# Kernel tuning notes

Measured on AMD Instinct MI355X. Metric: run time of the kernel, lower is better.

## Reference

```python
import jax, jax.numpy as jnp
import numpy as np

B, S, D, H = 4, 2048, 768, 12
HD = D // H  # head_dim = 64
NEG = 1e10
EPS = 1e-5

def setup_inputs() -> dict:
    key = jax.random.key(0)
    k1, k2, k3 = jax.random.split(key, 3)
    return {
        "context": jax.random.normal(k1, (B, S, D), dtype=jnp.float32),
        "pad_mask": jnp.ones((B, S), dtype=jnp.float32),
        "w_qkv": jax.random.normal(k2, (D, 3 * D), dtype=jnp.float32) * 0.02,
        "w_proj": jax.random.normal(k3, (D, D), dtype=jnp.float32) * (0.02 / np.sqrt(2.0 * 12)),
        "b_proj": jnp.zeros((D,), dtype=jnp.float32),
        "gamma": jnp.ones((D,), dtype=jnp.float32),
        "beta": jnp.zeros((D,), dtype=jnp.float32),
    }

def reference(context, pad_mask, w_qkv, w_proj, b_proj, gamma, beta):
    b, s, d = context.shape
    resid = context
    qkv = context @ w_qkv                       # [B,S,3D]
    q, k, v = jnp.split(qkv, 3, axis=-1)
    # [B,S,D] -> [B,H,S,HD]
    q = q.reshape(b, s, H, HD).transpose(0, 2, 1, 3)
    k = k.reshape(b, s, H, HD).transpose(0, 2, 1, 3)
    v = v.reshape(b, s, H, HD).transpose(0, 2, 1, 3)
    scores = jnp.einsum("bhqd,bhkd->bhqk", q, k) * (1.0 / np.sqrt(HD))
    m = pad_mask[:, None, None, :]              # [B,1,1,S]
    scores = scores * m - (1.0 - m) * NEG       # multiplicative mask + big negative
    attn = jax.nn.softmax(scores, axis=-1)      # dropout is identity at inference
    out = jnp.einsum("bhqk,bhkd->bhqd", attn, v)
    out = out.transpose(0, 2, 1, 3).reshape(b, s, d)
    out = out @ w_proj + b_proj
    x = out + resid
    mu = jnp.mean(x, axis=-1, keepdims=True)
    var = jnp.var(x, axis=-1, keepdims=True)
    return (x - mu) * jax.lax.rsqrt(var + EPS) * gamma + beta
```

## Files before the change

kernel.cpp:

```cpp
#include <hip/hip_runtime.h>

#define BB 4
#define SS 2048
#define DD 768
#define HH 12
#define HDD 64
#define BS (BB*SS)
#define NQKV (3*DD)
#define NEL (BS*DD)

typedef __attribute__((ext_vector_type(8))) __bf16 bf16x8;
typedef __attribute__((ext_vector_type(4))) float fx4;
typedef __attribute__((ext_vector_type(4))) int   ix4;

#define MFMA16(a,b,c) __builtin_amdgcn_mfma_f32_16x16x32_bf16((a),(b),(c),0,0,0)

#define GLLDS(g, l) __builtin_amdgcn_global_load_lds( \
    (const __attribute__((address_space(1))) void*)(g), \
    (__attribute__((address_space(3))) void*)(l), 16, 0, 0)

__device__ __forceinline__ unsigned short f2bf(float f) {
  unsigned u = __builtin_bit_cast(unsigned, f);
  u = (u + 0x7FFFu + ((u >> 16) & 1u)) >> 16;
  return (unsigned short)u;
}
__device__ __forceinline__ unsigned pkbf(float a, float b) {
  unsigned ua = __builtin_bit_cast(unsigned, a);
  unsigned ub = __builtin_bit_cast(unsigned, b);
  return ((ua + 0x8000u) >> 16) | ((ub + 0x8000u) & 0xFFFF0000u);
}
__device__ __forceinline__ unsigned cvtpk(float a, float b) {
  unsigned r;
  asm("v_cvt_pk_bf16_f32 %0, %1, %2" : "=v"(r) : "v"(a), "v"(b));
  return r;
}
__device__ __forceinline__ float ex2(float x) { return __builtin_amdgcn_exp2f(x); }

__global__ __launch_bounds__(256) void pack_bf16(const float* __restrict__ x,
                                                 unsigned short* __restrict__ y, int n4) {
  int i = blockIdx.x * 256 + threadIdx.x;
  if (i < n4) {
    float4 v = ((const float4*)x)[i];
    ((uint2*)y)[i] = make_uint2(pkbf(v.x, v.y), pkbf(v.z, v.w));
  }
}

__global__ __launch_bounds__(256) void mask_coef_k(const float* __restrict__ m,
                                                   float* __restrict__ ka,
                                                   float* __restrict__ kb, int n) {
  int i = blockIdx.x * 256 + threadIdx.x;
  if (i < n) {
    float v = m[i];
    ka[i] = v * 0.18033688f;
    kb[i] = __builtin_fmaf(v, 1.44269504e10f, -1.44269504e10f);
  }
}

__global__ __launch_bounds__(256) void pack_transpose(const float* __restrict__ w,
                                                      unsigned short* __restrict__ wT,
                                                      int K, int N) {
  __shared__ unsigned short t[32][33];
  int n0 = blockIdx.x * 32, k0 = blockIdx.y * 32;
  int tx = threadIdx.x & 31, ty = threadIdx.x >> 5;
#pragma unroll
  for (int r = ty; r < 32; r += 8)
    t[tx][r] = f2bf(w[(size_t)(k0 + r) * N + n0 + tx]);
  __syncthreads();
#pragma unroll
  for (int r = ty; r < 32; r += 8)
    wT[(size_t)(n0 + r) * K + k0 + tx] = t[r][tx];
}

__global__ __launch_bounds__(256) void gemm_qkv_k(const unsigned short* __restrict__ Wt,
                                                  const unsigned short* __restrict__ X,
                                                  unsigned short* __restrict__ Qo,
                                                  unsigned short* __restrict__ Ko,
                                                  unsigned short* __restrict__ Vto) {
  __shared__ unsigned short As[2 * 128 * 32];
  __shared__ unsigned short Bs[2 * 128 * 32];
  const int tid = threadIdx.x;
  const int w = tid >> 6, lane = tid & 63, quad = lane >> 4, l16 = lane & 15;
  const int m0 = blockIdx.y << 7;
  const int n0 = blockIdx.x << 7;
  const int wm = (w & 1) * 64, wn = (w >> 1) * 64;
  fx4 acc[4][4];
#pragma unroll
  for (int i = 0; i < 4; ++i)
#pragma unroll
    for (int c = 0; c < 4; ++c) acc[i][c] = (fx4){0.f, 0.f, 0.f, 0.f};

  const int c0 = tid, c1 = 256 + tid;
  const unsigned short* Ag0 = Wt + (size_t)(m0 + (c0 >> 2)) * DD + (c0 & 3) * 8;
  const unsigned short* Ag1 = Wt + (size_t)(m0 + (c1 >> 2)) * DD + (c1 & 3) * 8;
  const unsigned short* Bg0 = X + (size_t)(n0 + (c0 >> 2)) * DD + (c0 & 3) * 8;
  const unsigned short* Bg1 = X + (size_t)(n0 + (c1 >> 2)) * DD + (c1 & 3) * 8;
  const int wb = w * 1024;

  GLLDS(Ag0, (char*)As + wb);
  GLLDS(Ag1, (char*)As + 4096 + wb);
  GLLDS(Bg0, (char*)Bs + wb);
  GLLDS(Bg1, (char*)Bs + 4096 + wb);
  int cur = 0;

  for (int k0 = 0; k0 < DD; k0 += 32) {
    __syncthreads();
    if (k0 + 32 < DD) {
      GLLDS(Ag0 + k0 + 32, (char*)As + (cur ^ 1) * 8192 + wb);
      GLLDS(Ag1 + k0 + 32, (char*)As + (cur ^ 1) * 8192 + 4096 + wb);
      GLLDS(Bg0 + k0 + 32, (char*)Bs + (cur ^ 1) * 8192 + wb);
      GLLDS(Bg1 + k0 + 32, (char*)Bs + (cur ^ 1) * 8192 + 4096 + wb);
    }
    const unsigned short* Asc = As + cur * 4096;
    const unsigned short* Bsc = Bs + cur * 4096;
    bf16x8 af[4], bf[4];
#pragma unroll
    for (int i = 0; i < 4; ++i) af[i] = *(const bf16x8*)&Asc[(wm + i * 16 + l16) * 32 + quad * 8];
#pragma unroll
    for (int c = 0; c < 4; ++c) bf[c] = *(const bf16x8*)&Bsc[(wn + c * 16 + l16) * 32 + quad * 8];
#pragma unroll
    for (int i = 0; i < 4; ++i)
#pragma unroll
      for (int c = 0; c < 4; ++c) acc[i][c] = MFMA16(af[i], bf[c], acc[i][c]);
    cur ^= 1;
  }

  const int which = m0 / DD;
#pragma unroll
  for (int i = 0; i < 4; ++i) {
    int fb = m0 + wm + i * 16 + quad * 4;
    int d = fb - which * DD;
    int h = d >> 6, hd = d & 63;
#pragma unroll
    for (int c = 0; c < 4; ++c) {
      int srow = n0 + wn + c * 16 + l16;
      int b = srow >> 11, s = srow & (SS - 1);
      if (which == 0) {
        uint2 v = make_uint2(pkbf(acc[i][c][0], acc[i][c][1]), pkbf(acc[i][c][2], acc[i][c][3]));
        *(uint2*)&Qo[((size_t)(b * HH + h) * SS + s) * HDD + hd] = v;
      } else if (which == 1) {
        uint2 v = make_uint2(pkbf(acc[i][c][0], acc[i][c][1]), pkbf(acc[i][c][2], acc[i][c][3]));
        *(uint2*)&Ko[((size_t)(b * HH + h) * SS + s) * HDD + hd] = v;
      } else {
#pragma unroll
        for (int r = 0; r < 4; ++r)
          Vto[((size_t)(b * HH + h) * HDD + hd + r) * SS + s] = f2bf(acc[i][c][r]);
      }
    }
  }
}

__global__ __launch_bounds__(256) void gemm_proj_k(const unsigned short* __restrict__ Wt,
                                                   const unsigned short* __restrict__ X,
                                                   const float* __restrict__ ctx,
                                                   const float* __restrict__ bproj,
                                                   float* __restrict__ xf) {
  __shared__ unsigned short As[2 * 128 * 32];
  __shared__ unsigned short Bs[2 * 128 * 32];
  const int tid = threadIdx.x;
  const int w = tid >> 6, lane = tid & 63, quad = lane >> 4, l16 = lane & 15;
  const int m0 = blockIdx.y << 7;
  const int n0 = blockIdx.x << 7;
  const int wm = (w & 1) * 64, wn = (w >> 1) * 64;
  fx4 acc[4][4];
#pragma unroll
  for (int i = 0; i < 4; ++i)
#pragma unroll
    for (int c = 0; c < 4; ++c) acc[i][c] = (fx4){0.f, 0.f, 0.f, 0.f};

  const int c0 = tid, c1 = 256 + tid;
  const unsigned short* Ag0 = Wt + (size_t)(m0 + (c0 >> 2)) * DD + (c0 & 3) * 8;
  const unsigned short* Ag1 = Wt + (size_t)(m0 + (c1 >> 2)) * DD + (c1 & 3) * 8;
  const unsigned short* Bg0 = X + (size_t)(n0 + (c0 >> 2)) * DD + (c0 & 3) * 8;
  const unsigned short* Bg1 = X + (size_t)(n0 + (c1 >> 2)) * DD + (c1 & 3) * 8;
  const int wb = w * 1024;

  GLLDS(Ag0, (char*)As + wb);
  GLLDS(Ag1, (char*)As + 4096 + wb);
  GLLDS(Bg0, (char*)Bs + wb);
  GLLDS(Bg1, (char*)Bs + 4096 + wb);
  int cur = 0;

  for (int k0 = 0; k0 < DD; k0 += 32) {
    __syncthreads();
    if (k0 + 32 < DD) {
      GLLDS(Ag0 + k0 + 32, (char*)As + (cur ^ 1) * 8192 + wb);
      GLLDS(Ag1 + k0 + 32, (char*)As + (cur ^ 1) * 8192 + 4096 + wb);
      GLLDS(Bg0 + k0 + 32, (char*)Bs + (cur ^ 1) * 8192 + wb);
      GLLDS(Bg1 + k0 + 32, (char*)Bs + (cur ^ 1) * 8192 + 4096 + wb);
    }
    const unsigned short* Asc = As + cur * 4096;
    const unsigned short* Bsc = Bs + cur * 4096;
    bf16x8 af[4], bf[4];
#pragma unroll
    for (int i = 0; i < 4; ++i) af[i] = *(const bf16x8*)&Asc[(wm + i * 16 + l16) * 32 + quad * 8];
#pragma unroll
    for (int c = 0; c < 4; ++c) bf[c] = *(const bf16x8*)&Bsc[(wn + c * 16 + l16) * 32 + quad * 8];
#pragma unroll
    for (int i = 0; i < 4; ++i)
#pragma unroll
      for (int c = 0; c < 4; ++c) acc[i][c] = MFMA16(af[i], bf[c], acc[i][c]);
    cur ^= 1;
  }

#pragma unroll
  for (int i = 0; i < 4; ++i) {
    int fb = m0 + wm + i * 16 + quad * 4;
    float4 bp = *(const float4*)&bproj[fb];
#pragma unroll
    for (int c = 0; c < 4; ++c) {
      int srow = n0 + wn + c * 16 + l16;
      float4 cx = *(const float4*)&ctx[(size_t)srow * DD + fb];
      float4 r;
      r.x = acc[i][c][0] + bp.x + cx.x;
      r.y = acc[i][c][1] + bp.y + cx.y;
      r.z = acc[i][c][2] + bp.z + cx.z;
      r.w = acc[i][c][3] + bp.w + cx.w;
      *(float4*)&xf[(size_t)srow * DD + fb] = r;
    }
  }
}

__global__ __launch_bounds__(256) void attn_k(const unsigned short* __restrict__ Q,
                                              const unsigned short* __restrict__ K,
                                              const unsigned short* __restrict__ Vt,
                                              const float* __restrict__ ka,
                                              const float* __restrict__ kb,
                                              unsigned short* __restrict__ O) {
  __shared__ unsigned short Ks[64 * 64];
  __shared__ unsigned short Vts[64 * 64];
  __shared__ float kaS[SS];
  __shared__ float kbS[SS];
  const int tid = threadIdx.x;
  const int w = tid >> 6, lane = tid & 63;
  const int quad = lane >> 4, l16 = lane & 15;
  const int bh = blockIdx.y;
  const int b = bh / HH, h = bh - b * HH;
  const int q0 = blockIdx.x << 7;
  const unsigned short* Qb = Q + (size_t)bh * (SS * HDD);
  const unsigned short* Kb = K + (size_t)bh * (SS * HDD);
  const unsigned short* Vtb = Vt + (size_t)bh * (SS * HDD);
  const float* ka_b = ka + b * SS;
  const float* kb_b = kb + b * SS;

#pragma unroll
  for (int i = 0; i < 2; ++i) {
    int idx = i * 256 + tid;
    ((float4*)kaS)[idx] = ((const float4*)ka_b)[idx];
    ((float4*)kbS)[idx] = ((const float4*)kb_b)[idx];
  }

  bf16x8 qf[2][2];
#pragma unroll
  for (int qi = 0; qi < 2; ++qi)
#pragma unroll
    for (int f = 0; f < 2; ++f)
      qf[qi][f] = *(const bf16x8*)&Qb[(size_t)(q0 + w * 32 + qi * 16 + l16) * HDD + f * 32 + quad * 8];

  fx4 o[2][4];
#pragma unroll
  for (int qi = 0; qi < 2; ++qi)
#pragma unroll
    for (int ht = 0; ht < 4; ++ht) o[qi][ht] = (fx4){0.f, 0.f, 0.f, 0.f};
  fx4 sacc[2];
  sacc[0] = (fx4){0.f, 0.f, 0.f, 0.f};
  sacc[1] = (fx4){0.f, 0.f, 0.f, 0.f};

  const ix4 one4 = (ix4){0x3F803F80, 0x3F803F80, 0x3F803F80, 0x3F803F80};
  const bf16x8 onesf = __builtin_bit_cast(bf16x8, one4);

  const int cA = tid, cB = 256 + tid;
  const int rA = cA >> 3, pA = (cA & 7) ^ (rA & 7);
  const int rB = cB >> 3, pB = (cB & 7) ^ (rB & 7);

  ix4 rk0 = *(const ix4*)&Kb[(size_t)rA * HDD + pA * 8];
  ix4 rk1 = *(const ix4*)&Kb[(size_t)rB * HDD + pB * 8];
  ix4 rv0 = *(const ix4*)&Vtb[(size_t)rA * SS + pA * 8];
  ix4 rv1 = *(const ix4*)&Vtb[(size_t)rB * SS + pB * 8];

  for (int k0 = 0; k0 < SS; k0 += 64) {
    __syncthreads();
    *(ix4*)((char*)Ks + cA * 16) = rk0;
    *(ix4*)((char*)Ks + cB * 16) = rk1;
    *(ix4*)((char*)Vts + cA * 16) = rv0;
    *(ix4*)((char*)Vts + cB * 16) = rv1;
    __syncthreads();
    if (k0 + 64 < SS) {
      int kn = k0 + 64;
      rk0 = *(const ix4*)&Kb[(size_t)(kn + rA) * HDD + pA * 8];
      rk1 = *(const ix4*)&Kb[(size_t)(kn + rB) * HDD + pB * 8];
      rv0 = *(const ix4*)&Vtb[(size_t)rA * SS + kn + pA * 8];
      rv1 = *(const ix4*)&Vtb[(size_t)rB * SS + kn + pB * 8];
    }

    float4 mqa[4], mqb[4];
#pragma unroll
    for (int kt = 0; kt < 4; ++kt) {
      mqa[kt] = *(const float4*)&kaS[k0 + kt * 16 + quad * 4];
      mqb[kt] = *(const float4*)&kbS[k0 + kt * 16 + quad * 4];
    }

    bf16x8 kf[4][2];
#pragma unroll
    for (int kt = 0; kt < 4; ++kt) {
      int row = kt * 16 + l16;
      int rx = row & 7;
#pragma unroll
      for (int f = 0; f < 2; ++f)
        kf[kt][f] = *(const bf16x8*)&Ks[row * 64 + ((f * 4 + quad) ^ rx) * 8];
    }
    bf16x8 vf[4][2];
#pragma unroll
    for (int ht = 0; ht < 4; ++ht) {
      int row = ht * 16 + l16;
      int rx = row & 7;
#pragma unroll
      for (int f = 0; f < 2; ++f) {
        int dc0 = (f * 4 + (quad >> 1)) ^ rx;
        int dc1 = (f * 4 + 2 + (quad >> 1)) ^ rx;
        uint2 lo = *(const uint2*)((const char*)Vts + row * 128 + dc0 * 16 + (quad & 1) * 8);
        uint2 hi = *(const uint2*)((const char*)Vts + row * 128 + dc1 * 16 + (quad & 1) * 8);
        ix4 vv = (ix4){(int)lo.x, (int)lo.y, (int)hi.x, (int)hi.y};
        vf[ht][f] = __builtin_bit_cast(bf16x8, vv);
      }
    }

#pragma unroll
    for (int qi = 0; qi < 2; ++qi) {
      unsigned pw[8];
#pragma unroll
      for (int kt = 0; kt < 4; ++kt) {
        fx4 s = (fx4){0.f, 0.f, 0.f, 0.f};
        s = MFMA16(kf[kt][0], qf[qi][0], s);
        s = MFMA16(kf[kt][1], qf[qi][1], s);
        const float* ma = (const float*)&mqa[kt];
        const float* mc = (const float*)&mqb[kt];
        float p0 = ex2(__builtin_fmaf(s[0], ma[0], mc[0]));
        float p1 = ex2(__builtin_fmaf(s[1], ma[1], mc[1]));
        float p2 = ex2(__builtin_fmaf(s[2], ma[2], mc[2]));
        float p3 = ex2(__builtin_fmaf(s[3], ma[3], mc[3]));
        pw[kt * 2]     = cvtpk(p0, p1);
        pw[kt * 2 + 1] = cvtpk(p2, p3);
      }
      ix4 pi0 = (ix4){(int)pw[0], (int)pw[1], (int)pw[2], (int)pw[3]};
      ix4 pi1 = (ix4){(int)pw[4], (int)pw[5], (int)pw[6], (int)pw[7]};
      bf16x8 pf0 = __builtin_bit_cast(bf16x8, pi0);
      bf16x8 pf1 = __builtin_bit_cast(bf16x8, pi1);
      sacc[qi] = MFMA16(onesf, pf0, sacc[qi]);
      sacc[qi] = MFMA16(onesf, pf1, sacc[qi]);
#pragma unroll
      for (int ht = 0; ht < 4; ++ht) {
        o[qi][ht] = MFMA16(vf[ht][0], pf0, o[qi][ht]);
        o[qi][ht] = MFMA16(vf[ht][1], pf1, o[qi][ht]);
      }
    }
  }

#pragma unroll
  for (int qi = 0; qi < 2; ++qi) {
    float inv = 1.f / fmaxf(sacc[qi][0], 1e-30f);
    int sq = q0 + w * 32 + qi * 16 + l16;
    unsigned short* orow = O + ((size_t)(b * SS + sq)) * DD + h * HDD;
#pragma unroll
    for (int ht = 0; ht < 4; ++ht) {
      uint2 v = make_uint2(pkbf(o[qi][ht][0] * inv, o[qi][ht][1] * inv),
                           pkbf(o[qi][ht][2] * inv, o[qi][ht][3] * inv));
      *(uint2*)&orow[ht * 16 + quad * 4] = v;
    }
  }
}

__global__ __launch_bounds__(256) void ln_k(const float* __restrict__ x,
                                            const float* __restrict__ gamma,
                                            const float* __restrict__ beta,
                                            float* __restrict__ out) {
  const int row = blockIdx.x;
  const float* xr = x + (size_t)row * DD;
  const int t = threadIdx.x;
  float v0 = xr[t], v1 = xr[t + 256], v2 = xr[t + 512];
  float s = v0 + v1 + v2;
  float ss = v0 * v0 + v1 * v1 + v2 * v2;
#pragma unroll
  for (int d = 32; d > 0; d >>= 1) {
    s += __shfl_down(s, d);
    ss += __shfl_down(ss, d);
  }
  __shared__ float sh[10];
  int wv = t >> 6, lane = t & 63;
  if (lane == 0) { sh[wv] = s; sh[4 + wv] = ss; }
  __syncthreads();
  if (t == 0) {
    float S = sh[0] + sh[1] + sh[2] + sh[3];
    float SSm = sh[4] + sh[5] + sh[6] + sh[7];
    float mu = S * (1.0f / DD);
    float var = SSm * (1.0f / DD) - mu * mu;
    sh[8] = mu;
    sh[9] = rsqrtf(var + 1e-5f);
  }
  __syncthreads();
  float mu = sh[8], rstd = sh[9];
  out[(size_t)row * DD + t]       = (v0 - mu) * rstd * gamma[t]       + beta[t];
  out[(size_t)row * DD + t + 256] = (v1 - mu) * rstd * gamma[t + 256] + beta[t + 256];
  out[(size_t)row * DD + t + 512] = (v2 - mu) * rstd * gamma[t + 512] + beta[t + 512];
}

extern "C" void kernel_launch(void* const* d_in, const int* in_sizes, int n_in,
                              void* d_out, int out_size, void* d_ws, size_t ws_size,
                              hipStream_t stream) {
  (void)in_sizes; (void)n_in; (void)out_size; (void)ws_size;
  const float* ctx   = (const float*)d_in[0];
  const float* mask  = (const float*)d_in[1];
  const float* wqkv  = (const float*)d_in[2];
  const float* wproj = (const float*)d_in[3];
  const float* bproj = (const float*)d_in[4];
  const float* gamma = (const float*)d_in[5];
  const float* beta  = (const float*)d_in[6];
  float* out = (float*)d_out;

  char* p = (char*)d_ws;
  unsigned short* Xbf = (unsigned short*)p; p += (size_t)NEL * 2;
  unsigned short* Qw  = (unsigned short*)p; p += (size_t)NEL * 2;
  unsigned short* Kw  = (unsigned short*)p; p += (size_t)NEL * 2;
  unsigned short* Vtw = (unsigned short*)p; p += (size_t)NEL * 2;
  unsigned short* Ao  = (unsigned short*)p; p += (size_t)NEL * 2;
  unsigned short* WqkvT  = (unsigned short*)p; p += (size_t)DD * NQKV * 2;
  unsigned short* WprojT = (unsigned short*)p; p += (size_t)DD * DD * 2;
  float* kaw = (float*)p; p += (size_t)BS * 4;
  float* kbw = (float*)p; p += (size_t)BS * 4;
  float* xf = (float*)Qw;

  pack_bf16<<<NEL / 4 / 256, 256, 0, stream>>>(ctx, Xbf, NEL / 4);
  mask_coef_k<<<BS / 256, 256, 0, stream>>>(mask, kaw, kbw, BS);
  pack_transpose<<<dim3(NQKV / 32, DD / 32), 256, 0, stream>>>(wqkv, WqkvT, DD, NQKV);
  pack_transpose<<<dim3(DD / 32, DD / 32), 256, 0, stream>>>(wproj, WprojT, DD, DD);
  gemm_qkv_k<<<dim3(BS / 128, NQKV / 128), 256, 0, stream>>>(WqkvT, Xbf, Qw, Kw, Vtw);
  attn_k<<<dim3(SS / 128, BB * HH), 256, 0, stream>>>(Qw, Kw, Vtw, kaw, kbw, Ao);
  gemm_proj_k<<<dim3(BS / 128, DD / 128), 256, 0, stream>>>(WprojT, Ao, ctx, bproj, xf);
  ln_k<<<BS, 256, 0, stream>>>(xf, gamma, beta, out);
}
```

Before: 252.3 us.

## Merge prep kernels, fold mask coefficients into attention, swizzle GEMM blocks, per-wave layernorm

Three separate pack/transpose launches become one prep kernel, and the mask coefficient kernel is removed by computing those coefficients inside the attention kernel. Both GEMMs remap block indices so neighbouring tiles land on the same XCD, which is meant to improve L2 reuse. LayerNorm now handles one row per wave with float4 loads and xor shuffles, removing shared memory and block barriers. Together these cut launch count and synchronisation overhead, at the cost of a larger, branchier prep kernel and an integer-division remap in the GEMMs.

```diff
diff --git a/kernel.cpp b/kernel.cpp
--- a/kernel.cpp
+++ b/kernel.cpp
@@ -36,32 +36,36 @@
 }
 __device__ __forceinline__ float ex2(float x) { return __builtin_amdgcn_exp2f(x); }
 
-__global__ __launch_bounds__(256) void pack_bf16(const float* __restrict__ x,
-                                                 unsigned short* __restrict__ y, int n4) {
-  int i = blockIdx.x * 256 + threadIdx.x;
-  if (i < n4) {
-    float4 v = ((const float4*)x)[i];
-    ((uint2*)y)[i] = make_uint2(pkbf(v.x, v.y), pkbf(v.z, v.w));
-  }
-}
-
-__global__ __launch_bounds__(256) void mask_coef_k(const float* __restrict__ m,
-                                                   float* __restrict__ ka,
-                                                   float* __restrict__ kb, int n) {
-  int i = blockIdx.x * 256 + threadIdx.x;
-  if (i < n) {
-    float v = m[i];
-    ka[i] = v * 0.18033688f;
-    kb[i] = __builtin_fmaf(v, 1.44269504e10f, -1.44269504e10f);
-  }
-}
-
-__global__ __launch_bounds__(256) void pack_transpose(const float* __restrict__ w,
-                                                      unsigned short* __restrict__ wT,
-                                                      int K, int N) {
+#define PREP_PACK   6144
+#define PREP_TQKV   1728
+#define PREP_TPROJ  576
+__global__ __launch_bounds__(256) void prep_k(const float* __restrict__ ctx,
+                                              unsigned short* __restrict__ Xbf,
+                                              const float* __restrict__ wqkv,
+                                              unsigned short* __restrict__ WqkvT,
+                                              const float* __restrict__ wproj,
+                                              unsigned short* __restrict__ WprojT) {
   __shared__ unsigned short t[32][33];
-  int n0 = blockIdx.x * 32, k0 = blockIdx.y * 32;
-  int tx = threadIdx.x & 31, ty = threadIdx.x >> 5;
+  const int bid = blockIdx.x;
+  const int tid = threadIdx.x;
+  if (bid < PREP_PACK) {
+    int i = bid * 256 + tid;
+    float4 v = ((const float4*)ctx)[i];
+    ((uint2*)Xbf)[i] = make_uint2(pkbf(v.x, v.y), pkbf(v.z, v.w));
+    return;
+  }
+  const float* w; unsigned short* wT; int K, N, bx, by;
+  if (bid < PREP_PACK + PREP_TQKV) {
+    int tix = bid - PREP_PACK;
+    w = wqkv; wT = WqkvT; K = DD; N = NQKV;
+    bx = tix % 72; by = tix / 72;
+  } else {
+    int tix = bid - PREP_PACK - PREP_TQKV;
+    w = wproj; wT = WprojT; K = DD; N = DD;
+    bx = tix % 24; by = tix / 24;
+  }
+  int n0 = bx * 32, k0 = by * 32;
+  int tx = tid & 31, ty = tid >> 5;
 #pragma unroll
   for (int r = ty; r < 32; r += 8)
     t[tx][r] = f2bf(w[(size_t)(k0 + r) * N + n0 + tx]);
@@ -69,6 +73,15 @@
 #pragma unroll
   for (int r = ty; r < 32; r += 8)
     wT[(size_t)(n0 + r) * K + k0 + tx] = t[r][tx];
+}
+
+__device__ __forceinline__ void xcd_swz(int gx, int* bx, int* by) {
+  int nwg = gx * gridDim.y;
+  int flat = blockIdx.y * gx + blockIdx.x;
+  int cpx = nwg >> 3;
+  int swz = (flat & 7) * cpx + (flat >> 3);
+  *bx = swz % gx;
+  *by = swz / gx;
 }
 
 __global__ __launch_bounds__(256) void gemm_qkv_k(const unsigned short* __restrict__ Wt,
@@ -80,8 +93,9 @@
   __shared__ unsigned short Bs[2 * 128 * 32];
   const int tid = threadIdx.x;
   const int w = tid >> 6, lane = tid & 63, quad = lane >> 4, l16 = lane & 15;
-  const int m0 = blockIdx.y << 7;
-  const int n0 = blockIdx.x << 7;
+  int bx, by; xcd_swz(gridDim.x, &bx, &by);
+  const int m0 = by << 7;
+  const int n0 = bx << 7;
   const int wm = (w & 1) * 64, wn = (w >> 1) * 64;
   fx4 acc[4][4];
 #pragma unroll
@@ -158,8 +172,9 @@
   __shared__ unsigned short Bs[2 * 128 * 32];
   const int tid = threadIdx.x;
   const int w = tid >> 6, lane = tid & 63, quad = lane >> 4, l16 = lane & 15;
-  const int m0 = blockIdx.y << 7;
-  const int n0 = blockIdx.x << 7;
+  int bx, by; xcd_swz(gridDim.x, &bx, &by);
+  const int m0 = by << 7;
+  const int n0 = bx << 7;
   const int wm = (w & 1) * 64, wn = (w >> 1) * 64;
   fx4 acc[4][4];
 #pragma unroll
@@ -223,8 +238,7 @@
 __global__ __launch_bounds__(256) void attn_k(const unsigned short* __restrict__ Q,
                                               const unsigned short* __restrict__ K,
                                               const unsigned short* __restrict__ Vt,
-                                              const float* __restrict__ ka,
-                                              const float* __restrict__ kb,
+                                              const float* __restrict__ mask,
                                               unsigned short* __restrict__ O) {
   __shared__ unsigned short Ks[64 * 64];
   __shared__ unsigned short Vts[64 * 64];
@@ -239,14 +253,21 @@
   const unsigned short* Qb = Q + (size_t)bh * (SS * HDD);
   const unsigned short* Kb = K + (size_t)bh * (SS * HDD);
   const unsigned short* Vtb = Vt + (size_t)bh * (SS * HDD);
-  const float* ka_b = ka + b * SS;
-  const float* kb_b = kb + b * SS;
+  const float* mb = mask + b * SS;
 
 #pragma unroll
   for (int i = 0; i < 2; ++i) {
     int idx = i * 256 + tid;
-    ((float4*)kaS)[idx] = ((const float4*)ka_b)[idx];
-    ((float4*)kbS)[idx] = ((const float4*)kb_b)[idx];
+    float4 mv = ((const float4*)mb)[idx];
+    float4 a, c;
+    a.x = mv.x * 0.18033688f; a.y = mv.y * 0.18033688f;
+    a.z = mv.z * 0.18033688f; a.w = mv.w * 0.18033688f;
+    c.x = __builtin_fmaf(mv.x, 1.44269504e10f, -1.44269504e10f);
+    c.y = __builtin_fmaf(mv.y, 1.44269504e10f, -1.44269504e10f);
+    c.z = __builtin_fmaf(mv.z, 1.44269504e10f, -1.44269504e10f);
+    c.w = __builtin_fmaf(mv.w, 1.44269504e10f, -1.44269504e10f);
+    ((float4*)kaS)[idx] = a;
+    ((float4*)kbS)[idx] = c;
   }
 
   bf16x8 qf[2][2];
@@ -373,34 +394,36 @@
                                             const float* __restrict__ gamma,
                                             const float* __restrict__ beta,
                                             float* __restrict__ out) {
-  const int row = blockIdx.x;
+  const int wv = threadIdx.x >> 6, lane = threadIdx.x & 63;
+  const int row = blockIdx.x * 4 + wv;
   const float* xr = x + (size_t)row * DD;
-  const int t = threadIdx.x;
-  float v0 = xr[t], v1 = xr[t + 256], v2 = xr[t + 512];
-  float s = v0 + v1 + v2;
-  float ss = v0 * v0 + v1 * v1 + v2 * v2;
-#pragma unroll
-  for (int d = 32; d > 0; d >>= 1) {
-    s += __shfl_down(s, d);
-    ss += __shfl_down(ss, d);
-  }
-  __shared__ float sh[10];
-  int wv = t >> 6, lane = t & 63;
-  if (lane == 0) { sh[wv] = s; sh[4 + wv] = ss; }
-  __syncthreads();
-  if (t == 0) {
-    float S = sh[0] + sh[1] + sh[2] + sh[3];
-    float SSm = sh[4] + sh[5] + sh[6] + sh[7];
-    float mu = S * (1.0f / DD);
-    float var = SSm * (1.0f / DD) - mu * mu;
-    sh[8] = mu;
-    sh[9] = rsqrtf(var + 1e-5f);
-  }
-  __syncthreads();
-  float mu = sh[8], rstd = sh[9];
-  out[(size_t)row * DD + t]       = (v0 - mu) * rstd * gamma[t]       + beta[t];
-  out[(size_t)row * DD + t + 256] = (v1 - mu) * rstd * gamma[t + 256] + beta[t + 256];
-  out[(size_t)row * DD + t + 512] = (v2 - mu) * rstd * gamma[t + 512] + beta[t + 512];
+  float4 v[3];
+  float s = 0.f, ss = 0.f;
+#pragma unroll
+  for (int j = 0; j < 3; ++j) {
+    v[j] = *(const float4*)&xr[j * 256 + lane * 4];
+    s += v[j].x + v[j].y + v[j].z + v[j].w;
+    ss += v[j].x * v[j].x + v[j].y * v[j].y + v[j].z * v[j].z + v[j].w * v[j].w;
+  }
+#pragma unroll
+  for (int d = 1; d < 64; d <<= 1) {
+    s += __shfl_xor(s, d);
+    ss += __shfl_xor(ss, d);
+  }
+  float mu = s * (1.0f / DD);
+  float rstd = rsqrtf(ss * (1.0f / DD) - mu * mu + 1e-5f);
+  float* orow = out + (size_t)row * DD;
+#pragma unroll
+  for (int j = 0; j < 3; ++j) {
+    float4 g = *(const float4*)&gamma[j * 256 + lane * 4];
+    float4 be = *(const float4*)&beta[j * 256 + lane * 4];
+    float4 r;
+    r.x = (v[j].x - mu) * rstd * g.x + be.x;
+    r.y = (v[j].y - mu) * rstd * g.y + be.y;
+    r.z = (v[j].z - mu) * rstd * g.z + be.z;
+    r.w = (v[j].w - mu) * rstd * g.w + be.w;
+    *(float4*)&orow[j * 256 + lane * 4] = r;
+  }
 }
 
 extern "C" void kernel_launch(void* const* d_in, const int* in_sizes, int n_in,
@@ -424,16 +447,12 @@
   unsigned short* Ao  = (unsigned short*)p; p += (size_t)NEL * 2;
   unsigned short* WqkvT  = (unsigned short*)p; p += (size_t)DD * NQKV * 2;
   unsigned short* WprojT = (unsigned short*)p; p += (size_t)DD * DD * 2;
-  float* kaw = (float*)p; p += (size_t)BS * 4;
-  float* kbw = (float*)p; p += (size_t)BS * 4;
   float* xf = (float*)Qw;
 
-  pack_bf16<<<NEL / 4 / 256, 256, 0, stream>>>(ctx, Xbf, NEL / 4);
-  mask_coef_k<<<BS / 256, 256, 0, stream>>>(mask, kaw, kbw, BS);
-  pack_transpose<<<dim3(NQKV / 32, DD / 32), 256, 0, stream>>>(wqkv, WqkvT, DD, NQKV);
-  pack_transpose<<<dim3(DD / 32, DD / 32), 256, 0, stream>>>(wproj, WprojT, DD, DD);
+  prep_k<<<PREP_PACK + PREP_TQKV + PREP_TPROJ, 256, 0, stream>>>(
+      ctx, Xbf, wqkv, WqkvT, wproj, WprojT);
   gemm_qkv_k<<<dim3(BS / 128, NQKV / 128), 256, 0, stream>>>(WqkvT, Xbf, Qw, Kw, Vtw);
-  attn_k<<<dim3(SS / 128, BB * HH), 256, 0, stream>>>(Qw, Kw, Vtw, kaw, kbw, Ao);
+  attn_k<<<dim3(SS / 128, BB * HH), 256, 0, stream>>>(Qw, Kw, Vtw, mask, Ao);
   gemm_proj_k<<<dim3(BS / 128, DD / 128), 256, 0, stream>>>(WprojT, Ao, ctx, bproj, xf);
-  ln_k<<<BS, 256, 0, stream>>>(xf, gamma, beta, out);
-}
+  ln_k<<<BS / 4, 256, 0, stream>>>(xf, gamma, beta, out);
+}
```

New measurement: 254.7 us. Within noise of the previous version (+1.0%).
